# Performance work log

Hardware: AMD Instinct MI355X
Metric: run time of the kernel (lower is better)

Reference implementation:

```python
import jax, jax.numpy as jnp
import numpy as np

N = 500000      # total nodes
B = 10000       # number of graphs
D = 256         # node_size == global_size
SLOPE = 0.01    # LeakyReLU negative slope (torch default)

def leaky_relu(x):
    return jnp.where(x >= 0, x, SLOPE * x)

def setup_inputs() -> dict:
    key = jax.random.key(0)
    ks = jax.random.split(key, 10)
    xg_old = jax.random.normal(ks[0], (B, D), dtype=jnp.float32)
    x = jax.random.normal(ks[1], (N, D), dtype=jnp.float32)
    batch = jnp.sort(jax.random.randint(ks[2], (N,), 0, B)).astype(jnp.int64)
    s = 1.0 / np.sqrt(D)
    W_gate = jax.random.uniform(ks[3], (D, 1), minval=-s, maxval=s, dtype=jnp.float32)
    b_gate = jax.random.uniform(ks[4], (1,), minval=-s, maxval=s, dtype=jnp.float32)
    W_feat = jax.random.uniform(ks[5], (D, D), minval=-s, maxval=s, dtype=jnp.float32)
    b_feat = jax.random.uniform(ks[6], (D,), minval=-s, maxval=s, dtype=jnp.float32)
    s2 = 1.0 / np.sqrt(2 * D)
    W_t = jax.random.uniform(ks[7], (2 * D, D), minval=-s2, maxval=s2, dtype=jnp.float32)
    b_t = jax.random.uniform(ks[8], (D,), minval=-s2, maxval=s2, dtype=jnp.float32)
    return {"xg_old": xg_old, "x": x, "batch": batch,
            "W_gate": W_gate, "b_gate": b_gate,
            "W_feat": W_feat, "b_feat": b_feat,
            "W_t": W_t, "b_t": b_t}

def reference(xg_old, x, batch, W_gate, b_gate, W_feat, b_feat, W_t, b_t):
    batch = batch.astype(jnp.int32)
    # AttentionalAggregation: per-graph softmax over gate scores, weighted sum of feats
    gate = x @ W_gate + b_gate                               # [N, 1]
    feat = leaky_relu(x @ W_feat + b_feat)                   # [N, D]
    m = jax.ops.segment_max(gate, batch, num_segments=B)     # [B, 1]
    g = jnp.exp(gate - m[batch])                             # stable exp
    s = jax.ops.segment_sum(g, batch, num_segments=B)        # [B, 1]
    alpha = g / s[batch]                                     # [N, 1]
    xg = jax.ops.segment_sum(alpha * feat, batch, num_segments=B)  # [B, D]
    # concat with old global state, transform, residual
    cat = jnp.concatenate([xg, xg_old], axis=1)              # [B, 2D]
    out = leaky_relu(cat @ W_t + b_t) + xg_old               # [B, D]
    return out
```

## Files before the change

kernel.cpp:

```cpp
#include <hip/hip_runtime.h>
#include <hip/hip_bf16.h>
#include <math.h>

#define D 256
#define FT_STRIDE 72

typedef short v8s __attribute__((ext_vector_type(8)));
typedef float f32x4 __attribute__((ext_vector_type(4)));

__device__ __forceinline__ unsigned short f2b(float f) {
    return __bfloat16_as_ushort(__float2bfloat16(f));
}
__device__ __forceinline__ float b2f(unsigned short u) {
    return __bfloat162float(__ushort_as_bfloat16(u));
}

__global__ void segstart_kernel(const int* __restrict__ batch, int* __restrict__ seg_start,
                                int N, int B) {
    int b = blockIdx.x * blockDim.x + threadIdx.x;
    if (b > B) return;
    int lo = 0, hi = N;
    while (lo < hi) {
        int mid = (lo + hi) >> 1;
        if (batch[mid] < b) lo = mid + 1; else hi = mid;
    }
    seg_start[b] = lo;
}

template<bool CONV>
__global__ __launch_bounds__(256) void gate_conv_kernel(
    const float* __restrict__ x, const float* __restrict__ Wg,
    const float* __restrict__ bg, float* __restrict__ gate,
    unsigned short* __restrict__ xb16, int N) {
    const int lane = threadIdx.x & 63;
    const int wid = blockIdx.x * 4 + (threadIdx.x >> 6);
    const int nw = gridDim.x * 4;
    const float4 wv = *(const float4*)(Wg + lane * 4);
    const float bgv = bg[0];
    for (int n = wid; n < N; n += nw) {
        const float4 xv = *(const float4*)(x + (size_t)n * D + lane * 4);
        if (CONV) {
            ushort4 h = { f2b(xv.x), f2b(xv.y), f2b(xv.z), f2b(xv.w) };
            *(ushort4*)(xb16 + (size_t)n * D + lane * 4) = h;
        }
        float d = xv.x * wv.x + xv.y * wv.y + xv.z * wv.z + xv.w * wv.w;
        #pragma unroll
        for (int off = 32; off; off >>= 1) d += __shfl_xor(d, off, 64);
        if (lane == 0) gate[n] = d + bgv;
    }
}

__global__ __launch_bounds__(256) void stats_kernel(const float* __restrict__ gate,
                                                    const int* __restrict__ seg_start,
                                                    float* __restrict__ mvec,
                                                    float* __restrict__ invs, int B) {
    int wid = blockIdx.x * 4 + (threadIdx.x >> 6);
    int lane = threadIdx.x & 63;
    if (wid >= B) return;
    int s0 = seg_start[wid], s1 = seg_start[wid + 1];
    float m = -INFINITY;
    for (int i = s0 + lane; i < s1; i += 64) m = fmaxf(m, gate[i]);
    #pragma unroll
    for (int off = 32; off > 0; off >>= 1) m = fmaxf(m, __shfl_xor(m, off, 64));
    float s = 0.f;
    for (int i = s0 + lane; i < s1; i += 64) s += __expf(gate[i] - m);
    #pragma unroll
    for (int off = 32; off > 0; off >>= 1) s += __shfl_xor(s, off, 64);
    if (lane == 0) { mvec[wid] = m; invs[wid] = (s > 0.f) ? 1.f / s : 0.f; }
}

__global__ void wconv_kernel(const float* __restrict__ Wf, unsigned short* __restrict__ Wb,
                             int K) {
    int idx = blockIdx.x * 256 + threadIdx.x;
    int k = idx >> 8, n = idx & 255;
    if (k >= K) return;
    int n_tile = n >> 4, k_step = k >> 5, ksteps = K >> 5;
    int lane = ((k >> 3) & 3) * 16 + (n & 15);
    int j = k & 7;
    int dst = (((n_tile * ksteps + k_step) * 64) + lane) * 8 + j;
    Wb[dst] = f2b(Wf[k * 256 + n]);
}

template<bool BF16IN>
__global__ __launch_bounds__(256) void feat_attn_kernel(
    const float* __restrict__ x, const unsigned short* __restrict__ xb16,
    const unsigned short* __restrict__ Wb,
    const float* __restrict__ bfeat, const float* __restrict__ gate,
    const int* __restrict__ batch, const float* __restrict__ mvec,
    const float* __restrict__ invs, float* __restrict__ xg, int N) {

    __shared__ unsigned short feat_s[256 * FT_STRIDE] __attribute__((aligned(16)));
    __shared__ float alpha_s[64];
    __shared__ int batch_s[64];

    const int tid = threadIdx.x;
    const int n0 = blockIdx.x * 64;
    const int cnt = min(64, N - n0);

    if (tid < 64) {
        if (tid < cnt) {
            int n = n0 + tid;
            int b = batch[n];
            batch_s[tid] = b;
            alpha_s[tid] = __expf(gate[n] - mvec[b]) * invs[b];
        } else { batch_s[tid] = -1; alpha_s[tid] = 0.f; }
    }

    const int w = tid >> 6, lane = tid & 63;
    const int mrow = lane & 15, q = lane >> 4;

    f32x4 acc[4][4];
    #pragma unroll
    for (int i = 0; i < 4; i++)
        #pragma unroll
        for (int j = 0; j < 4; j++) acc[i][j] = (f32x4){0.f, 0.f, 0.f, 0.f};

    size_t rowbase[4];
    #pragma unroll
    for (int rb = 0; rb < 4; rb++) {
        int r = n0 + rb * 16 + mrow;
        if (r > N - 1) r = N - 1;
        rowbase[rb] = (size_t)r * D + q * 8;
    }

    v8s a_cur[4], b_cur[4], a_nxt[4], b_nxt[4];
    #pragma unroll
    for (int rb = 0; rb < 4; rb++)
        a_cur[rb] = *(const v8s*)(xb16 + rowbase[rb]);
    #pragma unroll
    for (int cb = 0; cb < 4; cb++)
        b_cur[cb] = *(const v8s*)(Wb + (((size_t)(w * 4 + cb) * 8 + 0) * 64 + lane) * 8);

    #pragma unroll
    for (int ks = 0; ks < 8; ks++) {
        if (ks < 7) {
            #pragma unroll
            for (int rb = 0; rb < 4; rb++)
                a_nxt[rb] = *(const v8s*)(xb16 + rowbase[rb] + (ks + 1) * 32);
            #pragma unroll
            for (int cb = 0; cb < 4; cb++)
                b_nxt[cb] = *(const v8s*)(Wb + (((size_t)(w * 4 + cb) * 8 + ks + 1) * 64 + lane) * 8);
        }
        #pragma unroll
        for (int rb = 0; rb < 4; rb++)
            #pragma unroll
            for (int cb = 0; cb < 4; cb++)
                acc[rb][cb] = __builtin_amdgcn_mfma_f32_16x16x32_bf16(
                    a_cur[rb], b_cur[cb], acc[rb][cb], 0, 0, 0);
        #pragma unroll
        for (int i = 0; i < 4; i++) { a_cur[i] = a_nxt[i]; b_cur[i] = b_nxt[i]; }
    }

    #pragma unroll
    for (int cb = 0; cb < 4; cb++) {
        int col = w * 64 + cb * 16 + mrow;
        float bias = bfeat[col];
        #pragma unroll
        for (int rb = 0; rb < 4; rb++) {
            ushort4 h;
            float y0 = acc[rb][cb][0] + bias; y0 = (y0 >= 0.f) ? y0 : 0.01f * y0;
            float y1 = acc[rb][cb][1] + bias; y1 = (y1 >= 0.f) ? y1 : 0.01f * y1;
            float y2 = acc[rb][cb][2] + bias; y2 = (y2 >= 0.f) ? y2 : 0.01f * y2;
            float y3 = acc[rb][cb][3] + bias; y3 = (y3 >= 0.f) ? y3 : 0.01f * y3;
            h.x = f2b(y0); h.y = f2b(y1); h.z = f2b(y2); h.w = f2b(y3);
            *(ushort4*)(&feat_s[col * FT_STRIDE + rb * 16 + q * 4]) = h;
        }
    }
    __syncthreads();

    float sum = 0.f;
    int cur = batch_s[0];
    for (int i0 = 0; i0 < cnt; i0 += 8) {
        v8s f = *(const v8s*)(&feat_s[tid * FT_STRIDE + i0]);
        #pragma unroll
        for (int j = 0; j < 8; j++) {
            int i = i0 + j;
            if (i >= cnt) break;
            int b = batch_s[i];
            if (b != cur) {
                atomicAdd(&xg[(size_t)cur * D + tid], sum);
                sum = 0.f; cur = b;
            }
            sum = fmaf(alpha_s[i], b2f((unsigned short)f[j]), sum);
        }
    }
    atomicAdd(&xg[(size_t)cur * D + tid], sum);
}

__global__ __launch_bounds__(256) void out_mfma_kernel(
    const float* __restrict__ xg, const float* __restrict__ xg_old,
    const unsigned short* __restrict__ Wtb, const float* __restrict__ bt,
    float* __restrict__ out, int B) {
    const int tid = threadIdx.x;
    const int w = tid >> 6, lane = tid & 63, mrow = lane & 15, q = lane >> 4;
    const int r0 = blockIdx.x * 64;

    f32x4 acc[4][4];
    #pragma unroll
    for (int i = 0; i < 4; i++)
        #pragma unroll
        for (int j = 0; j < 4; j++) acc[i][j] = (f32x4){0.f, 0.f, 0.f, 0.f};

    size_t rowbase[4];
    #pragma unroll
    for (int rb = 0; rb < 4; rb++) {
        int r = r0 + rb * 16 + mrow;
        if (r > B - 1) r = B - 1;
        rowbase[rb] = (size_t)r * D + q * 8;
    }

    #pragma unroll
    for (int ks = 0; ks < 16; ks++) {
        v8s a[4], bfr[4];
        #pragma unroll
        for (int rb = 0; rb < 4; rb++) {
            const float* src = (ks < 8) ? (xg + rowbase[rb] + ks * 32)
                                        : (xg_old + rowbase[rb] + (ks - 8) * 32);
            float4 f0 = *(const float4*)src;
            float4 f1 = *(const float4*)(src + 4);
            v8s v;
            v[0] = (short)f2b(f0.x); v[1] = (short)f2b(f0.y);
            v[2] = (short)f2b(f0.z); v[3] = (short)f2b(f0.w);
            v[4] = (short)f2b(f1.x); v[5] = (short)f2b(f1.y);
            v[6] = (short)f2b(f1.z); v[7] = (short)f2b(f1.w);
            a[rb] = v;
        }
        #pragma unroll
        for (int cb = 0; cb < 4; cb++)
            bfr[cb] = *(const v8s*)(Wtb + (((size_t)(w * 4 + cb) * 16 + ks) * 64 + lane) * 8);
        #pragma unroll
        for (int rb = 0; rb < 4; rb++)
            #pragma unroll
            for (int cb = 0; cb < 4; cb++)
                acc[rb][cb] = __builtin_amdgcn_mfma_f32_16x16x32_bf16(
                    a[rb], bfr[cb], acc[rb][cb], 0, 0, 0);
    }

    #pragma unroll
    for (int cb = 0; cb < 4; cb++) {
        int col = w * 64 + cb * 16 + mrow;
        float bias = bt[col];
        #pragma unroll
        for (int rb = 0; rb < 4; rb++) {
            #pragma unroll
            for (int reg = 0; reg < 4; reg++) {
                int row = r0 + rb * 16 + q * 4 + reg;
                if (row < B) {
                    float y = acc[rb][cb][reg] + bias;
                    y = (y >= 0.f) ? y : 0.01f * y;
                    out[(size_t)row * D + col] = y + xg_old[(size_t)row * D + col];
                }
            }
        }
    }
}

__global__ __launch_bounds__(256) void out_kernel(
    const float* __restrict__ xg, const float* __restrict__ xg_old,
    const float* __restrict__ Wt, const float* __restrict__ bt,
    float* __restrict__ out) {
    const int t = threadIdx.x;
    const int r0 = blockIdx.x * 8;
    float acc[8];
    #pragma unroll
    for (int r = 0; r < 8; r++) acc[r] = 0.f;
    for (int k = 0; k < D; k++) {
        const float w = Wt[k * D + t];
        #pragma unroll
        for (int r = 0; r < 8; r++)
            acc[r] = fmaf(xg[(size_t)(r0 + r) * D + k], w, acc[r]);
    }
    for (int k = 0; k < D; k++) {
        const float w = Wt[(D + k) * D + t];
        #pragma unroll
        for (int r = 0; r < 8; r++)
            acc[r] = fmaf(xg_old[(size_t)(r0 + r) * D + k], w, acc[r]);
    }
    const float btt = bt[t];
    #pragma unroll
    for (int r = 0; r < 8; r++) {
        float y = acc[r] + btt;
        y = (y >= 0.f) ? y : 0.01f * y;
        out[(size_t)(r0 + r) * D + t] = y + xg_old[(size_t)(r0 + r) * D + t];
    }
}

extern "C" void kernel_launch(void* const* d_in, const int* in_sizes, int n_in,
                              void* d_out, int out_size, void* d_ws, size_t ws_size,
                              hipStream_t stream) {
    const float* xg_old = (const float*)d_in[0];
    const float* x      = (const float*)d_in[1];
    const int*   batch  = (const int*)d_in[2];
    const float* W_gate = (const float*)d_in[3];
    const float* b_gate = (const float*)d_in[4];
    const float* W_feat = (const float*)d_in[5];
    const float* b_feat = (const float*)d_in[6];
    const float* W_t    = (const float*)d_in[7];
    const float* b_t    = (const float*)d_in[8];
    float* out = (float*)d_out;

    const int N = in_sizes[1] / D;
    const int B = in_sizes[0] / D;

    char* ws = (char*)d_ws;
    int*            seg_start = (int*)ws;
    float*          gate      = (float*)(ws + 0x10000);
    float*          mvec      = (float*)(ws + 0x220000);
    float*          invs      = (float*)(ws + 0x230000);
    unsigned short* Wb        = (unsigned short*)(ws + 0x240000);
    unsigned short* Wtb       = (unsigned short*)(ws + 0x260000);
    float*          xg        = (float*)(ws + 0x2A0000);
    unsigned short* xb16      = (unsigned short*)(ws + 0xCA0000);

    const size_t need_full = 0xCA0000 + (size_t)N * D * 2;
    const size_t need_mid  = 0xCA0000;
    const bool full = ws_size >= need_full;
    const bool mid  = ws_size >= need_mid;

    segstart_kernel<<<(B + 1 + 255) / 256, 256, 0, stream>>>(batch, seg_start, N, B);
    if (full)
        gate_conv_kernel<true><<<2048, 256, 0, stream>>>(x, W_gate, b_gate, gate, xb16, N);
    else
        gate_conv_kernel<false><<<2048, 256, 0, stream>>>(x, W_gate, b_gate, gate, xb16, N);
    stats_kernel<<<(B + 3) / 4, 256, 0, stream>>>(gate, seg_start, mvec, invs, B);
    wconv_kernel<<<256, 256, 0, stream>>>(W_feat, Wb, 256);
    if (mid) wconv_kernel<<<512, 256, 0, stream>>>(W_t, Wtb, 512);
    hipMemsetAsync(xg, 0, (size_t)B * D * sizeof(float), stream);

    if (full)
        feat_attn_kernel<true><<<(N + 63) / 64, 256, 0, stream>>>(
            x, xb16, Wb, b_feat, gate, batch, mvec, invs, xg, N);
    else
        feat_attn_kernel<false><<<(N + 63) / 64, 256, 0, stream>>>(
            x, xb16, Wb, b_feat, gate, batch, mvec, invs, xg, N);

    if (mid)
        out_mfma_kernel<<<(B + 63) / 64, 256, 0, stream>>>(xg, xg_old, Wtb, b_t, out, B);
    else
        out_kernel<<<B / 8, 256, 0, stream>>>(xg, xg_old, W_t, b_t, out);
}
```

Before: 1.015 ms.

## Fuse prep kernels, switch feat GEMM to 32x32 MFMA, fold alpha into epilogue

Merges segment-start search, the two weight conversions and the xg zeroing into one prep launch. The feature GEMM moves from 16x16x32 to 32x32x16 bf16 MFMA tiles with a new weight layout and triple-buffered A loads. Alpha is now applied in the epilogue before the bf16 store, so the reduction only sums, with a fast path when eight rows share a graph. The gate kernel handles two rows per iteration. These cut launch overhead and reduction work, at the cost of different bf16 rounding and some hardcoded sizes (block counts, the 640000 zero length).

Result: faster. 952.2 us (-6.2%).

```diff
diff --git a/kernel.cpp b/kernel.cpp
--- a/kernel.cpp
+++ b/kernel.cpp
@@ -7,6 +7,7 @@
 
 typedef short v8s __attribute__((ext_vector_type(8)));
 typedef float f32x4 __attribute__((ext_vector_type(4)));
+typedef float f32x16 __attribute__((ext_vector_type(16)));
 
 __device__ __forceinline__ unsigned short f2b(float f) {
     return __bfloat16_as_ushort(__float2bfloat16(f));
@@ -15,16 +16,37 @@
     return __bfloat162float(__ushort_as_bfloat16(u));
 }
 
-__global__ void segstart_kernel(const int* __restrict__ batch, int* __restrict__ seg_start,
-                                int N, int B) {
-    int b = blockIdx.x * blockDim.x + threadIdx.x;
-    if (b > B) return;
-    int lo = 0, hi = N;
-    while (lo < hi) {
-        int mid = (lo + hi) >> 1;
-        if (batch[mid] < b) lo = mid + 1; else hi = mid;
-    }
-    seg_start[b] = lo;
+__global__ void prep_kernel(const int* __restrict__ batch, int* __restrict__ seg_start,
+                            const float* __restrict__ Wf, unsigned short* __restrict__ Wb32,
+                            const float* __restrict__ Wt, unsigned short* __restrict__ Wtb,
+                            float* __restrict__ xg, int N, int B) {
+    const int blk = blockIdx.x, tid = threadIdx.x;
+    if (blk < 40) {
+        int b = blk * 256 + tid;
+        if (b > B) return;
+        int lo = 0, hi = N;
+        while (lo < hi) {
+            int mid = (lo + hi) >> 1;
+            if (batch[mid] < b) lo = mid + 1; else hi = mid;
+        }
+        seg_start[b] = lo;
+    } else if (blk < 296) {
+        int idx = (blk - 40) * 256 + tid;
+        int k = idx >> 8, n = idx & 255;
+        int lane = ((k >> 3) & 1) * 32 + (n & 31);
+        int j = k & 7, kst = k >> 4, ntile = n >> 5;
+        Wb32[(((ntile * 16 + kst) * 64) + lane) * 8 + j] = f2b(Wf[k * 256 + n]);
+    } else if (blk < 808) {
+        int idx = (blk - 296) * 256 + tid;
+        int k = idx >> 8, n = idx & 255;
+        int ntile = n >> 4, kst = k >> 5;
+        int lane = ((k >> 3) & 3) * 16 + (n & 15);
+        int j = k & 7;
+        Wtb[(((ntile * 16 + kst) * 64) + lane) * 8 + j] = f2b(Wt[k * 256 + n]);
+    } else {
+        int idx = (blk - 808) * 256 + tid;
+        if (idx < 640000) ((float4*)xg)[idx] = make_float4(0.f, 0.f, 0.f, 0.f);
+    }
 }
 
 template<bool CONV>
@@ -37,16 +59,23 @@
     const int nw = gridDim.x * 4;
     const float4 wv = *(const float4*)(Wg + lane * 4);
     const float bgv = bg[0];
-    for (int n = wid; n < N; n += nw) {
-        const float4 xv = *(const float4*)(x + (size_t)n * D + lane * 4);
+    for (int n = wid * 2; n < N; n += nw * 2) {
+        const float4 xv0 = *(const float4*)(x + (size_t)n * D + lane * 4);
+        const float4 xv1 = *(const float4*)(x + (size_t)(n + 1) * D + lane * 4);
         if (CONV) {
-            ushort4 h = { f2b(xv.x), f2b(xv.y), f2b(xv.z), f2b(xv.w) };
-            *(ushort4*)(xb16 + (size_t)n * D + lane * 4) = h;
-        }
-        float d = xv.x * wv.x + xv.y * wv.y + xv.z * wv.z + xv.w * wv.w;
-        #pragma unroll
-        for (int off = 32; off; off >>= 1) d += __shfl_xor(d, off, 64);
-        if (lane == 0) gate[n] = d + bgv;
+            ushort4 h0 = { f2b(xv0.x), f2b(xv0.y), f2b(xv0.z), f2b(xv0.w) };
+            ushort4 h1 = { f2b(xv1.x), f2b(xv1.y), f2b(xv1.z), f2b(xv1.w) };
+            *(ushort4*)(xb16 + (size_t)n * D + lane * 4) = h0;
+            *(ushort4*)(xb16 + (size_t)(n + 1) * D + lane * 4) = h1;
+        }
+        float d0 = xv0.x * wv.x + xv0.y * wv.y + xv0.z * wv.z + xv0.w * wv.w;
+        float d1 = xv1.x * wv.x + xv1.y * wv.y + xv1.z * wv.z + xv1.w * wv.w;
+        #pragma unroll
+        for (int off = 32; off; off >>= 1) {
+            d0 += __shfl_xor(d0, off, 64);
+            d1 += __shfl_xor(d1, off, 64);
+        }
+        if (lane == 0) { gate[n] = d0 + bgv; gate[n + 1] = d1 + bgv; }
     }
 }
 
@@ -69,22 +98,10 @@
     if (lane == 0) { mvec[wid] = m; invs[wid] = (s > 0.f) ? 1.f / s : 0.f; }
 }
 
-__global__ void wconv_kernel(const float* __restrict__ Wf, unsigned short* __restrict__ Wb,
-                             int K) {
-    int idx = blockIdx.x * 256 + threadIdx.x;
-    int k = idx >> 8, n = idx & 255;
-    if (k >= K) return;
-    int n_tile = n >> 4, k_step = k >> 5, ksteps = K >> 5;
-    int lane = ((k >> 3) & 3) * 16 + (n & 15);
-    int j = k & 7;
-    int dst = (((n_tile * ksteps + k_step) * 64) + lane) * 8 + j;
-    Wb[dst] = f2b(Wf[k * 256 + n]);
-}
-
 template<bool BF16IN>
-__global__ __launch_bounds__(256) void feat_attn_kernel(
+__global__ __launch_bounds__(256, 4) void feat_attn_kernel(
     const float* __restrict__ x, const unsigned short* __restrict__ xb16,
-    const unsigned short* __restrict__ Wb,
+    const unsigned short* __restrict__ Wb32,
     const float* __restrict__ bfeat, const float* __restrict__ gate,
     const int* __restrict__ batch, const float* __restrict__ mvec,
     const float* __restrict__ invs, float* __restrict__ xg, int N) {
@@ -95,93 +112,143 @@
 
     const int tid = threadIdx.x;
     const int n0 = blockIdx.x * 64;
-    const int cnt = min(64, N - n0);
 
     if (tid < 64) {
-        if (tid < cnt) {
-            int n = n0 + tid;
+        int n = n0 + tid;
+        if (n < N) {
             int b = batch[n];
             batch_s[tid] = b;
             alpha_s[tid] = __expf(gate[n] - mvec[b]) * invs[b];
-        } else { batch_s[tid] = -1; alpha_s[tid] = 0.f; }
+        } else {
+            batch_s[tid] = batch[N - 1];
+            alpha_s[tid] = 0.f;
+        }
     }
 
     const int w = tid >> 6, lane = tid & 63;
-    const int mrow = lane & 15, q = lane >> 4;
-
-    f32x4 acc[4][4];
-    #pragma unroll
-    for (int i = 0; i < 4; i++)
-        #pragma unroll
-        for (int j = 0; j < 4; j++) acc[i][j] = (f32x4){0.f, 0.f, 0.f, 0.f};
-
-    size_t rowbase[4];
-    #pragma unroll
-    for (int rb = 0; rb < 4; rb++) {
-        int r = n0 + rb * 16 + mrow;
+    const int l31 = lane & 31, lh = lane >> 5;
+
+    f32x16 acc[2][2];
+    #pragma unroll
+    for (int i = 0; i < 2; i++)
+        #pragma unroll
+        for (int j = 0; j < 2; j++)
+            #pragma unroll
+            for (int e = 0; e < 16; e++) acc[i][j][e] = 0.f;
+
+    size_t abase[2];
+    #pragma unroll
+    for (int rt = 0; rt < 2; rt++) {
+        int r = n0 + rt * 32 + l31;
         if (r > N - 1) r = N - 1;
-        rowbase[rb] = (size_t)r * D + q * 8;
-    }
-
-    v8s a_cur[4], b_cur[4], a_nxt[4], b_nxt[4];
-    #pragma unroll
-    for (int rb = 0; rb < 4; rb++)
-        a_cur[rb] = *(const v8s*)(xb16 + rowbase[rb]);
-    #pragma unroll
-    for (int cb = 0; cb < 4; cb++)
-        b_cur[cb] = *(const v8s*)(Wb + (((size_t)(w * 4 + cb) * 8 + 0) * 64 + lane) * 8);
-
-    #pragma unroll
-    for (int ks = 0; ks < 8; ks++) {
-        if (ks < 7) {
-            #pragma unroll
-            for (int rb = 0; rb < 4; rb++)
-                a_nxt[rb] = *(const v8s*)(xb16 + rowbase[rb] + (ks + 1) * 32);
-            #pragma unroll
-            for (int cb = 0; cb < 4; cb++)
-                b_nxt[cb] = *(const v8s*)(Wb + (((size_t)(w * 4 + cb) * 8 + ks + 1) * 64 + lane) * 8);
-        }
-        #pragma unroll
-        for (int rb = 0; rb < 4; rb++)
-            #pragma unroll
-            for (int cb = 0; cb < 4; cb++)
-                acc[rb][cb] = __builtin_amdgcn_mfma_f32_16x16x32_bf16(
-                    a_cur[rb], b_cur[cb], acc[rb][cb], 0, 0, 0);
-        #pragma unroll
-        for (int i = 0; i < 4; i++) { a_cur[i] = a_nxt[i]; b_cur[i] = b_nxt[i]; }
-    }
-
-    #pragma unroll
-    for (int cb = 0; cb < 4; cb++) {
-        int col = w * 64 + cb * 16 + mrow;
+        abase[rt] = (size_t)r * D + lh * 8;
+    }
+
+    v8s A[3][2], Bf[2][2];
+    #pragma unroll
+    for (int p = 0; p < 2; p++) {
+        #pragma unroll
+        for (int rt = 0; rt < 2; rt++) {
+            if (BF16IN) A[p][rt] = *(const v8s*)(xb16 + abase[rt] + p * 16);
+            else {
+                const float* src = x + abase[rt] + p * 16;
+                float4 f0 = *(const float4*)src, f1 = *(const float4*)(src + 4);
+                v8s v; v[0]=(short)f2b(f0.x); v[1]=(short)f2b(f0.y);
+                v[2]=(short)f2b(f0.z); v[3]=(short)f2b(f0.w);
+                v[4]=(short)f2b(f1.x); v[5]=(short)f2b(f1.y);
+                v[6]=(short)f2b(f1.z); v[7]=(short)f2b(f1.w);
+                A[p][rt] = v;
+            }
+        }
+        #pragma unroll
+        for (int ct = 0; ct < 2; ct++)
+            Bf[p][ct] = *(const v8s*)(Wb32 + (((size_t)(w * 2 + ct) * 16 + p) * 64 + lane) * 8);
+    }
+
+    #pragma unroll
+    for (int ks = 0; ks < 16; ks++) {
+        const int cs = ks % 3, bs = ks & 1;
+        if (ks < 14) {
+            const int ns = (ks + 2) % 3;
+            #pragma unroll
+            for (int rt = 0; rt < 2; rt++) {
+                if (BF16IN) A[ns][rt] = *(const v8s*)(xb16 + abase[rt] + (ks + 2) * 16);
+                else {
+                    const float* src = x + abase[rt] + (ks + 2) * 16;
+                    float4 f0 = *(const float4*)src, f1 = *(const float4*)(src + 4);
+                    v8s v; v[0]=(short)f2b(f0.x); v[1]=(short)f2b(f0.y);
+                    v[2]=(short)f2b(f0.z); v[3]=(short)f2b(f0.w);
+                    v[4]=(short)f2b(f1.x); v[5]=(short)f2b(f1.y);
+                    v[6]=(short)f2b(f1.z); v[7]=(short)f2b(f1.w);
+                    A[ns][rt] = v;
+                }
+            }
+        }
+        if (ks < 15) {
+            const int nb = (ks + 1) & 1;
+            #pragma unroll
+            for (int ct = 0; ct < 2; ct++)
+                Bf[nb][ct] = *(const v8s*)(Wb32 + (((size_t)(w * 2 + ct) * 16 + ks + 1) * 64 + lane) * 8);
+        }
+        #pragma unroll
+        for (int rt = 0; rt < 2; rt++)
+            #pragma unroll
+            for (int ct = 0; ct < 2; ct++)
+                acc[rt][ct] = __builtin_amdgcn_mfma_f32_32x32x16_bf16(
+                    A[cs][rt], Bf[bs][ct], acc[rt][ct], 0, 0, 0);
+    }
+
+    __syncthreads();
+
+    #pragma unroll
+    for (int ct = 0; ct < 2; ct++) {
+        int col = w * 64 + ct * 32 + l31;
         float bias = bfeat[col];
         #pragma unroll
-        for (int rb = 0; rb < 4; rb++) {
-            ushort4 h;
-            float y0 = acc[rb][cb][0] + bias; y0 = (y0 >= 0.f) ? y0 : 0.01f * y0;
-            float y1 = acc[rb][cb][1] + bias; y1 = (y1 >= 0.f) ? y1 : 0.01f * y1;
-            float y2 = acc[rb][cb][2] + bias; y2 = (y2 >= 0.f) ? y2 : 0.01f * y2;
-            float y3 = acc[rb][cb][3] + bias; y3 = (y3 >= 0.f) ? y3 : 0.01f * y3;
-            h.x = f2b(y0); h.y = f2b(y1); h.z = f2b(y2); h.w = f2b(y3);
-            *(ushort4*)(&feat_s[col * FT_STRIDE + rb * 16 + q * 4]) = h;
+        for (int rt = 0; rt < 2; rt++) {
+            #pragma unroll
+            for (int g = 0; g < 4; g++) {
+                int rbase = rt * 32 + g * 8 + 4 * lh;
+                ushort4 h;
+                #pragma unroll
+                for (int rr = 0; rr < 4; rr++) {
+                    float y = acc[rt][ct][g * 4 + rr] + bias;
+                    y = (y >= 0.f) ? y : 0.01f * y;
+                    y *= alpha_s[rbase + rr];
+                    ((unsigned short*)&h)[rr] = f2b(y);
+                }
+                *(ushort4*)(&feat_s[col * FT_STRIDE + rbase]) = h;
+            }
         }
     }
     __syncthreads();
 
     float sum = 0.f;
     int cur = batch_s[0];
-    for (int i0 = 0; i0 < cnt; i0 += 8) {
+    #pragma unroll
+    for (int i0 = 0; i0 < 64; i0 += 8) {
         v8s f = *(const v8s*)(&feat_s[tid * FT_STRIDE + i0]);
-        #pragma unroll
-        for (int j = 0; j < 8; j++) {
-            int i = i0 + j;
-            if (i >= cnt) break;
-            int b = batch_s[i];
-            if (b != cur) {
+        int b0 = batch_s[i0], b7 = batch_s[i0 + 7];
+        if (b0 == b7) {
+            if (b0 != cur) {
                 atomicAdd(&xg[(size_t)cur * D + tid], sum);
-                sum = 0.f; cur = b;
-            }
-            sum = fmaf(alpha_s[i], b2f((unsigned short)f[j]), sum);
+                sum = 0.f; cur = b0;
+            }
+            float p0 = b2f((unsigned short)f[0]) + b2f((unsigned short)f[1]);
+            float p1 = b2f((unsigned short)f[2]) + b2f((unsigned short)f[3]);
+            float p2 = b2f((unsigned short)f[4]) + b2f((unsigned short)f[5]);
+            float p3 = b2f((unsigned short)f[6]) + b2f((unsigned short)f[7]);
+            sum += (p0 + p1) + (p2 + p3);
+        } else {
+            #pragma unroll
+            for (int j = 0; j < 8; j++) {
+                int b = batch_s[i0 + j];
+                if (b != cur) {
+                    atomicAdd(&xg[(size_t)cur * D + tid], sum);
+                    sum = 0.f; cur = b;
+                }
+                sum += b2f((unsigned short)f[j]);
+            }
         }
     }
     atomicAdd(&xg[(size_t)cur * D + tid], sum);
@@ -252,36 +319,6 @@
                 }
             }
         }
-    }
-}
-
-__global__ __launch_bounds__(256) void out_kernel(
-    const float* __restrict__ xg, const float* __restrict__ xg_old,
-    const float* __restrict__ Wt, const float* __restrict__ bt,
-    float* __restrict__ out) {
-    const int t = threadIdx.x;
-    const int r0 = blockIdx.x * 8;
-    float acc[8];
-    #pragma unroll
-    for (int r = 0; r < 8; r++) acc[r] = 0.f;
-    for (int k = 0; k < D; k++) {
-        const float w = Wt[k * D + t];
-        #pragma unroll
-        for (int r = 0; r < 8; r++)
-            acc[r] = fmaf(xg[(size_t)(r0 + r) * D + k], w, acc[r]);
-    }
-    for (int k = 0; k < D; k++) {
-        const float w = Wt[(D + k) * D + t];
-        #pragma unroll
-        for (int r = 0; r < 8; r++)
-            acc[r] = fmaf(xg_old[(size_t)(r0 + r) * D + k], w, acc[r]);
-    }
-    const float btt = bt[t];
-    #pragma unroll
-    for (int r = 0; r < 8; r++) {
-        float y = acc[r] + btt;
-        y = (y >= 0.f) ? y : 0.01f * y;
-        out[(size_t)(r0 + r) * D + t] = y + xg_old[(size_t)(r0 + r) * D + t];
     }
 }
 
@@ -307,35 +344,27 @@
     float*          gate      = (float*)(ws + 0x10000);
     float*          mvec      = (float*)(ws + 0x220000);
     float*          invs      = (float*)(ws + 0x230000);
-    unsigned short* Wb        = (unsigned short*)(ws + 0x240000);
+    unsigned short* Wb32      = (unsigned short*)(ws + 0x240000);
     unsigned short* Wtb       = (unsigned short*)(ws + 0x260000);
     float*          xg        = (float*)(ws + 0x2A0000);
     unsigned short* xb16      = (unsigned short*)(ws + 0xCA0000);
 
     const size_t need_full = 0xCA0000 + (size_t)N * D * 2;
-    const size_t need_mid  = 0xCA0000;
     const bool full = ws_size >= need_full;
-    const bool mid  = ws_size >= need_mid;
-
-    segstart_kernel<<<(B + 1 + 255) / 256, 256, 0, stream>>>(batch, seg_start, N, B);
+
+    prep_kernel<<<3308, 256, 0, stream>>>(batch, seg_start, W_feat, Wb32, W_t, Wtb, xg, N, B);
     if (full)
         gate_conv_kernel<true><<<2048, 256, 0, stream>>>(x, W_gate, b_gate, gate, xb16, N);
     else
         gate_conv_kernel<false><<<2048, 256, 0, stream>>>(x, W_gate, b_gate, gate, xb16, N);
     stats_kernel<<<(B + 3) / 4, 256, 0, stream>>>(gate, seg_start, mvec, invs, B);
-    wconv_kernel<<<256, 256, 0, stream>>>(W_feat, Wb, 256);
-    if (mid) wconv_kernel<<<512, 256, 0, stream>>>(W_t, Wtb, 512);
-    hipMemsetAsync(xg, 0, (size_t)B * D * sizeof(float), stream);
 
     if (full)
         feat_attn_kernel<true><<<(N + 63) / 64, 256, 0, stream>>>(
-            x, xb16, Wb, b_feat, gate, batch, mvec, invs, xg, N);
+            x, xb16, Wb32, b_feat, gate, batch, mvec, invs, xg, N);
     else
         feat_attn_kernel<false><<<(N + 63) / 64, 256, 0, stream>>>(
-            x, xb16, Wb, b_feat, gate, batch, mvec, invs, xg, N);
-
-    if (mid)
-        out_mfma_kernel<<<(B + 63) / 64, 256, 0, stream>>>(xg, xg_old, Wtb, b_t, out, B);
-    else
-        out_kernel<<<B / 8, 256, 0, stream>>>(xg, xg_old, W_t, b_t, out);
-}
+            x, xb16, Wb32, b_feat, gate, batch, mvec, invs, xg, N);
+
+    out_mfma_kernel<<<(B + 63) / 64, 256, 0, stream>>>(xg, xg_old, Wtb, b_t, out, B);
+}
```
